# Kernel optimization log

Hardware: AMD Instinct MI355X
Metric: run time of the kernel (lower is better)

## Reference

```python
import jax, jax.numpy as jnp
import numpy as np

B, K, W, H = 32, 64, 100, 150
ALPHA = 0.2        # leaky-relu slope
THRES = 2e-4       # causal threshold


def setup_inputs() -> dict:
    ks = jax.random.split(jax.random.key(0), 20)
    s = 0.1
    inp = {
        "x": jax.random.normal(ks[0], (B, K, W), jnp.float32),
        "y": jax.random.normal(ks[1], (B, K, 1), jnp.float32),
        "z_noise": jax.random.normal(ks[2], (B, H), jnp.float32),
        "lin_w": jax.random.normal(ks[3], (W, W), jnp.float32) * s,
        "lin_b": jax.random.normal(ks[4], (W,), jnp.float32) * s,
        "a": jax.random.normal(ks[5], (2, 1), jnp.float32),
        "bias": jax.random.normal(ks[6], (K, K * W), jnp.float32) * 0.01,
        "gl_wih": jax.random.normal(ks[7], (3 * H, W), jnp.float32) * s,
        "gl_whh": jax.random.normal(ks[8], (3 * H, H), jnp.float32) * s,
        "gl_bih": jax.random.normal(ks[9], (3 * H,), jnp.float32) * s,
        "gl_bhh": jax.random.normal(ks[10], (3 * H,), jnp.float32) * s,
        "mu_w": jax.random.normal(ks[11], (H, H), jnp.float32) * s,
        "mu_b": jax.random.normal(ks[12], (H,), jnp.float32) * s,
        "std_w": jax.random.normal(ks[13], (H, H), jnp.float32) * s,
        "std_b": jax.random.normal(ks[14], (H,), jnp.float32) * s,
        "net_wih": jax.random.normal(ks[15], (K, 3 * H, W), jnp.float32) * s,
        "net_whh": jax.random.normal(ks[16], (K, 3 * H, H), jnp.float32) * s,
        "net_bih": jax.random.normal(ks[17], (K, 3 * H), jnp.float32) * s,
        "net_bhh": jax.random.normal(ks[18], (K, 3 * H), jnp.float32) * s,
    }
    return inp


def _gru_last(wih, whh, bih, bhh, xs, h0):
    # xs: [B, S, in], h0: [B, H] -> final hidden [B, H]. PyTorch gate order r,z,n.
    gx = jnp.einsum('bsi,gi->sbg', xs, wih) + bih  # [S, B, 3H]
    h_dim = h0.shape[-1]

    def step(h, g):
        gh = h @ whh.T + bhh
        r = jax.nn.sigmoid(g[:, :h_dim] + gh[:, :h_dim])
        z = jax.nn.sigmoid(g[:, h_dim:2 * h_dim] + gh[:, h_dim:2 * h_dim])
        n = jnp.tanh(g[:, 2 * h_dim:] + r * gh[:, 2 * h_dim:])
        return (1.0 - z) * n + z * h, None

    h_last, _ = jax.lax.scan(step, h0, gx)
    return h_last


def reference(x, y, z_noise, lin_w, lin_b, a, bias, gl_wih, gl_whh, gl_bih, gl_bhh,
              mu_w, mu_b, std_w, std_b, net_wih, net_whh, net_bih, net_bhh):
    xw = x[:, :, -W:]
    Wx = xw @ lin_w.T + lin_b                       # [B, K, W]
    v = Wx.reshape(Wx.shape[0], K * W)              # [B, K*W]
    # e = a_input @ a, where a_input[...,0]=y broadcast, a_input[...,1]=v tiled per node
    e = a[0, 0] * y + a[1, 0] * v[:, None, :] + bias  # [B, K, K*W]
    e = jax.nn.leaky_relu(e, ALPHA)
    attention = jax.nn.softmax(e, axis=2)           # dropout p=0 -> identity
    A = attention >= THRES                           # [B, K, K*W] mask
    Ax = jnp.where(A, v[:, None, :], 0.0)
    cause_x = Wx + Ax.sum(axis=2, keepdims=True)    # [B, K, W]
    # left GRU over the node dimension (seq len = K)
    h0 = jnp.zeros((cause_x.shape[0], H), cause_x.dtype)
    h_t = _gru_last(gl_wih, gl_whh, gl_bih, gl_bhh, cause_x, h0)  # [B, H]
    mu = h_t @ mu_w.T + mu_b
    log_var = h_t @ std_w.T + std_b
    sigma = jnp.exp(0.5 * log_var)
    z = mu + sigma * z_noise                        # [B, H]
    # K independent GRUs, same input Wx and same init state z -> vmap over weights
    causes = jax.vmap(lambda wi, wh, bi, bh: _gru_last(wi, wh, bi, bh, Wx, z))(
        net_wih, net_whh, net_bih, net_bhh)         # [K, B, H]
    return causes.transpose(1, 0, 2)                # [B, K, H]
```

## Files before the change

kernel.cpp:

```cpp
#include <hip/hip_runtime.h>

#define Bc 32
#define Kc 64
#define Wc 100
#define Hc 150
#define H3c 450
#define KWc 6400
#define ALPHAc 0.2f
#define THRESc 0.0002f

typedef unsigned int u32;
typedef unsigned short u16;
typedef __attribute__((ext_vector_type(8))) short short8;
typedef __attribute__((ext_vector_type(4))) float floatx4;

#define OFF_WX      0u
#define OFF_CS      204800u
#define OFF_GX      206848u
#define OFF_HT      1128448u
#define OFF_Z       1133248u

__device__ __forceinline__ float us2f(u16 u){ u32 x=((u32)u)<<16; return __uint_as_float(x); }
__device__ __forceinline__ u16 f2us(float f){
  u32 x = __float_as_uint(f);
  u32 r = (x + 0x7fffu + ((x>>16)&1u)) >> 16;
  return (u16)r;
}

__device__ __forceinline__ void lds_barrier(){
  __builtin_amdgcn_sched_barrier(0);
  asm volatile("s_waitcnt lgkmcnt(0)" ::: "memory");
  __builtin_amdgcn_s_barrier();
  __builtin_amdgcn_sched_barrier(0);
}

__global__ void wx_kernel(const float* __restrict__ x, const float* __restrict__ lin_w,
                          const float* __restrict__ lin_b, float* __restrict__ ws){
  int o = blockIdx.x*256 + threadIdx.x;
  if (o >= Bc*KWc) return;
  int i = o % Wc;
  int bk = o / Wc;
  const float4* xr = (const float4*)(x + bk*Wc);
  const float4* wr = (const float4*)(lin_w + i*Wc);
  float acc = lin_b[i];
  #pragma unroll
  for (int j=0;j<25;j++){
    float4 xv = xr[j], wv = wr[j];
    acc += xv.x*wv.x + xv.y*wv.y + xv.z*wv.z + xv.w*wv.w;
  }
  ws[OFF_WX + o] = acc;
}

__global__ void attn_kernel(const float* __restrict__ y, const float* __restrict__ a,
                            const float* __restrict__ bias, float* __restrict__ ws){
  __shared__ __align__(16) float e_l[KWc];
  __shared__ float red[4];
  int row = blockIdx.x;
  int b = row >> 6, k = row & 63;
  int tid = threadIdx.x;
  float a0 = a[0], a1 = a[1];
  float yv = y[row];
  const float4* v4  = (const float4*)(ws + OFF_WX + (size_t)b*KWc);
  const float4* br4 = (const float4*)(bias + (size_t)k*KWc);
  float4* e4 = (float4*)e_l;
  float ay = a0*yv;
  float m = -3.4e38f;
  for (int j=tid; j<KWc/4; j+=256){
    float4 vv = v4[j], bb = br4[j];
    float4 e;
    e.x = ay + a1*vv.x + bb.x; e.x = (e.x>=0.f)?e.x:ALPHAc*e.x;
    e.y = ay + a1*vv.y + bb.y; e.y = (e.y>=0.f)?e.y:ALPHAc*e.y;
    e.z = ay + a1*vv.z + bb.z; e.z = (e.z>=0.f)?e.z:ALPHAc*e.z;
    e.w = ay + a1*vv.w + bb.w; e.w = (e.w>=0.f)?e.w:ALPHAc*e.w;
    e4[j] = e;
    m = fmaxf(m, fmaxf(fmaxf(e.x,e.y), fmaxf(e.z,e.w)));
  }
  for (int o=32;o;o>>=1) m = fmaxf(m, __shfl_down(m, o));
  if ((tid&63)==0) red[tid>>6] = m;
  __syncthreads();
  m = fmaxf(fmaxf(red[0],red[1]), fmaxf(red[2],red[3]));
  __syncthreads();
  float ssum = 0.f;
  for (int j=tid; j<KWc/4; j+=256){
    float4 e = e4[j];
    ssum += __expf(e.x-m) + __expf(e.y-m) + __expf(e.z-m) + __expf(e.w-m);
  }
  for (int o=32;o;o>>=1) ssum += __shfl_down(ssum, o);
  if ((tid&63)==0) red[tid>>6] = ssum;
  __syncthreads();
  float s = red[0]+red[1]+red[2]+red[3];
  float thr = m + logf(THRESc * s);
  float cs = 0.f;
  for (int j=tid; j<KWc/4; j+=256){
    float4 e = e4[j];
    float4 vv = v4[j];
    if (e.x >= thr) cs += vv.x;
    if (e.y >= thr) cs += vv.y;
    if (e.z >= thr) cs += vv.z;
    if (e.w >= thr) cs += vv.w;
  }
  for (int o=32;o;o>>=1) cs += __shfl_down(cs, o);
  if ((tid&63)==0) red[tid>>6] = cs;
  __syncthreads();
  if (tid==0) ws[OFF_CS + row] = red[0]+red[1]+red[2]+red[3];
}

__global__ void glproj_kernel(const float* __restrict__ gl_wih, const float* __restrict__ gl_bih,
                              float* __restrict__ ws){
  int o = blockIdx.x*256 + threadIdx.x;
  if (o >= Kc*Bc*H3c) return;
  int g = o % H3c;
  int t = o / H3c;
  int b = t & 31, s = t >> 5;
  float cs = ws[OFF_CS + b*Kc + s];
  const float4* xr = (const float4*)(ws + OFF_WX + b*KWc + s*Wc);
  const float4* wr = (const float4*)(gl_wih + g*Wc);
  float acc = gl_bih[g];
  #pragma unroll
  for (int j=0;j<25;j++){
    float4 wv = wr[j], xv = xr[j];
    acc += (xv.x+cs)*wv.x + (xv.y+cs)*wv.y + (xv.z+cs)*wv.z + (xv.w+cs)*wv.w;
  }
  ws[OFF_GX + o] = acc;
}

__global__ void __launch_bounds__(512,1) glgru4_kernel(
    const float* __restrict__ gl_whh, const float* __restrict__ gl_bhh,
    float* __restrict__ ws){
  __shared__ __align__(16) u16 bF[5*16*40];
  __shared__ float g_l[480*10];
  int b0 = blockIdx.x*8;
  int tid = threadIdx.x;
  int w = tid >> 6, lane = tid & 63, quad = lane >> 4, n16 = lane & 15;

  short8 whhA[4][5];
  #pragma unroll
  for (int ti=0; ti<4; ti++){
    int tile = w*4 + ti;
    int sec = tile/10;
    int sr = (tile - sec*10)*16 + n16;
    bool rowok = (tile < 30) && (sr < Hc);
    int grow = (sec<3 ? sec : 2)*Hc + sr;
    const float* wr = gl_whh + (size_t)grow*Hc;
    #pragma unroll
    for (int c=0;c<5;c++){
      union { short8 v; u16 u[8]; } t8;
      #pragma unroll
      for (int j2=0;j2<4;j2++){
        int kk2 = c*32 + quad*8 + j2*2;
        float2 wv = (rowok && (kk2+1) < Hc) ? *(const float2*)(wr + kk2) : make_float2(0.f,0.f);
        t8.u[j2*2]   = f2us(wv.x);
        t8.u[j2*2+1] = f2us(wv.y);
      }
      whhA[ti][c] = t8.v;
    }
  }
  for (int i=tid; i<5*16*40/2; i+=512) ((u32*)bF)[i] = 0u;

  float hst[3] = {0.f,0.f,0.f};
  float bh_r[3], bh_z[3], bh_n[3];
  int tT[3], tBL[3];
  #pragma unroll
  for (int q=0;q<3;q++){
    int task = tid + q*512;
    if (task < 1200){
      int bl = task/150, t = task - bl*150;
      tT[q] = t; tBL[q] = bl;
      bh_r[q] = gl_bhh[t];
      bh_z[q] = gl_bhh[Hc+t];
      bh_n[q] = gl_bhh[2*Hc+t];
    } else { tT[q] = 0; tBL[q] = -1; }
  }

  for (int s=0;s<Kc;s++){
    lds_barrier();
    float gxr[3], gxz[3], gxn[3];
    const float* gxb = ws + OFF_GX + (size_t)(s*Bc)*H3c;
    #pragma unroll
    for (int q=0;q<3;q++){
      if (tBL[q] >= 0){
        const float* gp = gxb + (size_t)(b0+tBL[q])*H3c;
        int t = tT[q];
        gxr[q] = gp[t]; gxz[q] = gp[Hc+t]; gxn[q] = gp[2*Hc+t];
      }
    }
    const u16* bBase = bF + (size_t)n16*40 + (size_t)quad*8;
    short8 bh[5];
    #pragma unroll
    for (int c=0;c<5;c++) bh[c] = *(const short8*)(bBase + (size_t)c*640);
    floatx4 acc[4] = {{0.f,0.f,0.f,0.f},{0.f,0.f,0.f,0.f},{0.f,0.f,0.f,0.f},{0.f,0.f,0.f,0.f}};
    #pragma unroll
    for (int c=0;c<5;c++){
      #pragma unroll
      for (int ti=0;ti<4;ti++)
        acc[ti] = __builtin_amdgcn_mfma_f32_16x16x32_bf16(whhA[ti][c], bh[c], acc[ti], 0,0,0);
    }
    #pragma unroll
    for (int ti=0;ti<4;ti++){
      #pragma unroll
      for (int r=0;r<4;r++) acc[ti][r] += __shfl_xor(acc[ti][r], 8);
    }
    if (n16 < 8){
      #pragma unroll
      for (int ti=0;ti<4;ti++){
        int tile = w*4 + ti;
        if (tile < 30){
          int row0 = tile*16 + quad*4;
          float* gp = g_l + row0*10 + n16;
          #pragma unroll
          for (int r=0;r<4;r++) gp[r*10] = acc[ti][r];
        }
      }
    }
    lds_barrier();
    float grv[3], gzv[3], gnv[3];
    #pragma unroll
    for (int q=0;q<3;q++){
      if (tBL[q] >= 0){
        int t = tT[q], bl = tBL[q];
        grv[q] = g_l[t*10+bl];
        gzv[q] = g_l[(160+t)*10+bl];
        gnv[q] = g_l[(320+t)*10+bl];
      }
    }
    #pragma unroll
    for (int q=0;q<3;q++){
      if (tBL[q] >= 0){
        int t = tT[q], bl = tBL[q];
        float a_r = gxr[q] + grv[q] + bh_r[q];
        float a_z = gxz[q] + gzv[q] + bh_z[q];
        float r  = 1.f/(1.f+__expf(-a_r));
        float zz = 1.f/(1.f+__expf(-a_z));
        float nx = gxn[q] + r*(gnv[q] + bh_n[q]);
        nx = fminf(fmaxf(nx,-15.f),15.f);
        float e2 = __expf(2.f*nx);
        float n = (e2-1.f)/(e2+1.f);
        float h = (1.f-zz)*n + zz*hst[q];
        hst[q] = h;
        u16 hi = f2us(h); float hif = us2f(hi); u16 lo = f2us(h - hif);
        bF[(t>>5)*640 + bl*40 + (t&31)] = hi;
        bF[(t>>5)*640 + (bl+8)*40 + (t&31)] = lo;
      }
    }
  }
  #pragma unroll
  for (int q=0;q<3;q++){
    if (tBL[q] >= 0)
      ws[OFF_HT + (size_t)(b0+tBL[q])*Hc + tT[q]] = hst[q];
  }
}

__global__ void z_kernel(const float* __restrict__ z_noise, const float* __restrict__ mu_w,
                         const float* __restrict__ mu_b, const float* __restrict__ std_w,
                         const float* __restrict__ std_b, float* __restrict__ ws){
  int o = blockIdx.x*256 + threadIdx.x;
  if (o >= Bc*Hc) return;
  int t = o % Hc, b = o / Hc;
  const float* h = ws + OFF_HT + b*Hc;
  const float2* mwr = (const float2*)(mu_w + t*Hc);
  const float2* swr = (const float2*)(std_w + t*Hc);
  float mu = mu_b[t], lv = std_b[t];
  for (int j=0;j<Hc/2;j++){
    float2 mw = mwr[j], sw = swr[j];
    float h0 = h[2*j], h1 = h[2*j+1];
    mu += h0*mw.x + h1*mw.y;
    lv += h0*sw.x + h1*sw.y;
  }
  float sg = expf(0.5f*lv);
  ws[OFF_Z + o] = mu + sg*z_noise[o];
}

__global__ void __launch_bounds__(512,1) causes3_kernel(
    const float* __restrict__ net_wih, const float* __restrict__ net_whh,
    const float* __restrict__ net_bih, const float* __restrict__ net_bhh,
    const float* __restrict__ ws, float* __restrict__ out){
  __shared__ __align__(16) u16 bF[9*16*40];
  __shared__ float g_rz[320*10];
  __shared__ float g_nh[160*10];
  __shared__ float g_np[160*10];
  int kk = blockIdx.x & 63, bg = blockIdx.x >> 6, b0 = bg*8;
  int tid = threadIdx.x;
  int w = tid >> 6, lane = tid & 63, quad = lane >> 4, n16 = lane & 15;
  const float* whhk = net_whh + (size_t)kk*H3c*Hc;
  const float* wihk = net_wih + (size_t)kk*H3c*Wc;
  const float* bihk = net_bih + kk*H3c;
  const float* bhhk = net_bhh + kk*H3c;

  short8 whhA[4][5], wihA[4][4];
  #pragma unroll
  for (int ti=0; ti<4; ti++){
    int tile = w*4 + ti;
    int sec = tile/10;
    int sr = (tile - sec*10)*16 + n16;
    bool rowok = (tile < 30) && (sr < Hc);
    int grow = (sec<3 ? sec : 2)*Hc + sr;
    #pragma unroll
    for (int c=0;c<5;c++){
      union { short8 v; u16 u[8]; } t8;
      #pragma unroll
      for (int j=0;j<8;j++){
        int k = c*32 + quad*8 + j;
        float v = (rowok && k < Hc) ? whhk[(size_t)grow*Hc + k] : 0.f;
        t8.u[j] = f2us(v);
      }
      whhA[ti][c] = t8.v;
    }
    #pragma unroll
    for (int c=0;c<4;c++){
      union { short8 v; u16 u[8]; } t8;
      #pragma unroll
      for (int j=0;j<8;j++){
        int k = c*32 + quad*8 + j;
        float v = (rowok && k < Wc) ? wihk[(size_t)grow*Wc + k] : 0.f;
        t8.u[j] = f2us(v);
      }
      wihA[ti][c] = t8.v;
    }
  }

  for (int i=tid; i<9*16*40/2; i+=512) ((u32*)bF)[i] = 0u;

  float hst[3] = {0.f,0.f,0.f};
  float brz_r[3], brz_z[3], bnh_[3], bnp_[3];
  #pragma unroll
  for (int q=0;q<3;q++){
    int task = tid + q*512;
    if (task < 1200){
      int t = task >> 3, bb = task & 7;
      float h = ws[OFF_Z + (b0+bb)*Hc + t];
      hst[q] = h;
      brz_r[q] = bhhk[t]      + bihk[t];
      brz_z[q] = bhhk[Hc+t]   + bihk[Hc+t];
      bnh_[q]  = bhhk[2*Hc+t];
      bnp_[q]  = bihk[2*Hc+t];
      u16 hi = f2us(h); float hif = us2f(hi); u16 lo = f2us(h - hif);
      bF[(t>>5)*640 + bb*40 + (t&31)] = hi;
      bF[(t>>5)*640 + (bb+8)*40 + (t&31)] = lo;
    }
  }
  for (int it=tid; it<800; it+=512){
    int bb = it/100, i = it - bb*100;
    float xv = ws[OFF_WX + (b0+bb)*KWc + i];
    bF[(5+(i>>5))*640 + bb*40 + (i&31)] = f2us(xv);
  }

  int bb0 = tid/100, i0 = tid - bb0*100;
  int it1 = tid + 512;
  int bb1 = it1/100, i1 = it1 - bb1*100;
  bool v1ok = (it1 < 800);

  const bool isN = (w >= 5);
  for (int s=0;s<Kc;s++){
    float xp0 = 0.f, xp1 = 0.f;
    if (s < Kc-1){
      xp0 = ws[OFF_WX + (size_t)(b0+bb0)*KWc + (s+1)*Wc + i0];
      if (v1ok) xp1 = ws[OFF_WX + (size_t)(b0+bb1)*KWc + (s+1)*Wc + i1];
    }
    lds_barrier();
    const u16* bBase = bF + (size_t)n16*40 + (size_t)quad*8;
    short8 bx[4];
    #pragma unroll
    for (int c=0;c<4;c++) bx[c] = *(const short8*)(bBase + (size_t)(5+c)*640);
    short8 bh[5];
    #pragma unroll
    for (int c=0;c<5;c++) bh[c] = *(const short8*)(bBase + (size_t)c*640);
    floatx4 acc[4] = {{0.f,0.f,0.f,0.f},{0.f,0.f,0.f,0.f},{0.f,0.f,0.f,0.f},{0.f,0.f,0.f,0.f}};
    #pragma unroll
    for (int ca=0;ca<4;ca++){
      #pragma unroll
      for (int ti=0;ti<4;ti++)
        acc[ti] = __builtin_amdgcn_mfma_f32_16x16x32_bf16(wihA[ti][ca], bx[ca], acc[ti], 0,0,0);
    }
    if (isN){
      if (n16 < 8){
        #pragma unroll
        for (int ti=0;ti<4;ti++){
          int tile = w*4 + ti;
          if (tile < 30){
            int srb = (tile - 20)*16 + quad*4;
            float* gq = g_np + srb*10 + n16;
            #pragma unroll
            for (int r=0;r<4;r++) gq[r*10] = acc[ti][r];
          }
        }
      }
      #pragma unroll
      for (int ti=0;ti<4;ti++) acc[ti] = (floatx4){0.f,0.f,0.f,0.f};
    }
    #pragma unroll
    for (int c=0;c<5;c++){
      #pragma unroll
      for (int ti=0;ti<4;ti++)
        acc[ti] = __builtin_amdgcn_mfma_f32_16x16x32_bf16(whhA[ti][c], bh[c], acc[ti], 0,0,0);
    }
    #pragma unroll
    for (int ti=0;ti<4;ti++){
      #pragma unroll
      for (int r=0;r<4;r++) acc[ti][r] += __shfl_xor(acc[ti][r], 8);
    }
    if (n16 < 8){
      #pragma unroll
      for (int ti=0;ti<4;ti++){
        int tile = w*4 + ti;
        if (tile < 30){
          int sec = tile/10;
          int srb = (tile - sec*10)*16 + quad*4;
          if (sec < 2){
            float* gp = g_rz + (sec*160 + srb)*10 + n16;
            #pragma unroll
            for (int r=0;r<4;r++) gp[r*10] = acc[ti][r];
          } else {
            float* gh = g_nh + srb*10 + n16;
            #pragma unroll
            for (int r=0;r<4;r++) gh[r*10] = acc[ti][r];
          }
        }
      }
    }
    lds_barrier();
    #pragma unroll
    for (int q=0;q<3;q++){
      int task = tid + q*512;
      if (task < 1200){
        int t = task >> 3, bb = task & 7;
        float a_r = g_rz[t*10+bb] + brz_r[q];
        float a_z = g_rz[(160+t)*10+bb] + brz_z[q];
        float r  = 1.f/(1.f+__expf(-a_r));
        float zz = 1.f/(1.f+__expf(-a_z));
        float nx = (g_np[t*10+bb] + bnp_[q]) + r*(g_nh[t*10+bb] + bnh_[q]);
        nx = fminf(fmaxf(nx,-15.f),15.f);
        float e2 = __expf(2.f*nx);
        float n = (e2-1.f)/(e2+1.f);
        float h = (1.f-zz)*n + zz*hst[q];
        hst[q] = h;
        u16 hi = f2us(h); float hif = us2f(hi); u16 lo = f2us(h - hif);
        bF[(t>>5)*640 + bb*40 + (t&31)] = hi;
        bF[(t>>5)*640 + (bb+8)*40 + (t&31)] = lo;
      }
    }
    if (s < Kc-1){
      bF[(5+(i0>>5))*640 + bb0*40 + (i0&31)] = f2us(xp0);
      if (v1ok) bF[(5+(i1>>5))*640 + bb1*40 + (i1&31)] = f2us(xp1);
    }
  }
  #pragma unroll
  for (int q=0;q<3;q++){
    int task = tid + q*512;
    if (task < 1200){
      int t = task >> 3, bb = task & 7;
      out[((size_t)(b0+bb)*Kc + kk)*Hc + t] = hst[q];
    }
  }
}

extern "C" void kernel_launch(void* const* d_in, const int* in_sizes, int n_in,
                              void* d_out, int out_size, void* d_ws, size_t ws_size,
                              hipStream_t stream){
  const float* x        = (const float*)d_in[0];
  const float* y        = (const float*)d_in[1];
  const float* z_noise  = (const float*)d_in[2];
  const float* lin_w    = (const float*)d_in[3];
  const float* lin_b    = (const float*)d_in[4];
  const float* a        = (const float*)d_in[5];
  const float* bias     = (const float*)d_in[6];
  const float* gl_wih   = (const float*)d_in[7];
  const float* gl_whh   = (const float*)d_in[8];
  const float* gl_bih   = (const float*)d_in[9];
  const float* gl_bhh   = (const float*)d_in[10];
  const float* mu_w     = (const float*)d_in[11];
  const float* mu_b     = (const float*)d_in[12];
  const float* std_w    = (const float*)d_in[13];
  const float* std_b    = (const float*)d_in[14];
  const float* net_wih  = (const float*)d_in[15];
  const float* net_whh  = (const float*)d_in[16];
  const float* net_bih  = (const float*)d_in[17];
  const float* net_bhh  = (const float*)d_in[18];
  float* ws = (float*)d_ws;
  float* out = (float*)d_out;

  wx_kernel<<<(Bc*KWc+255)/256, 256, 0, stream>>>(x, lin_w, lin_b, ws);
  attn_kernel<<<Bc*Kc, 256, 0, stream>>>(y, a, bias, ws);
  glproj_kernel<<<(Kc*Bc*H3c+255)/256, 256, 0, stream>>>(gl_wih, gl_bih, ws);
  glgru4_kernel<<<4, 512, 0, stream>>>(gl_whh, gl_bhh, ws);
  z_kernel<<<(Bc*Hc+255)/256, 256, 0, stream>>>(z_noise, mu_w, mu_b, std_w, std_b, ws);
  causes3_kernel<<<Kc*4, 512, 0, stream>>>(net_wih, net_whh, net_bih, net_bhh, ws, out);
}
```

Before: 488.7 us.

## Rewrite left GRU recurrence as one block per batch with register-resident weights

Replaces the 4-block MFMA-based left GRU, where each block handles 8 batches with hi/lo bf16 split hidden state, with 32 blocks of one batch each. Each of 450 threads keeps one bf16 row of W_hh packed in registers and computes its dot product against an fp32 hidden state held in double-buffered LDS. The aim is to spread the serial 64-step recurrence across more CUs and shorten the per-step critical path. In exchange, the matrix cores are no longer used, each thread carries 75 registers of weights, and the weight loads are repeated per batch.

```diff
diff --git a/kernel.cpp b/kernel.cpp
--- a/kernel.cpp
+++ b/kernel.cpp
@@ -127,127 +127,71 @@
 __global__ void __launch_bounds__(512,1) glgru4_kernel(
     const float* __restrict__ gl_whh, const float* __restrict__ gl_bhh,
     float* __restrict__ ws){
-  __shared__ __align__(16) u16 bF[5*16*40];
-  __shared__ float g_l[480*10];
-  int b0 = blockIdx.x*8;
+  __shared__ __align__(16) float hbuf[2][152];
+  __shared__ float dotb[3*152];
+  int b = blockIdx.x;
   int tid = threadIdx.x;
-  int w = tid >> 6, lane = tid & 63, quad = lane >> 4, n16 = lane & 15;
-
-  short8 whhA[4][5];
-  #pragma unroll
-  for (int ti=0; ti<4; ti++){
-    int tile = w*4 + ti;
-    int sec = tile/10;
-    int sr = (tile - sec*10)*16 + n16;
-    bool rowok = (tile < 30) && (sr < Hc);
-    int grow = (sec<3 ? sec : 2)*Hc + sr;
-    const float* wr = gl_whh + (size_t)grow*Hc;
-    #pragma unroll
-    for (int c=0;c<5;c++){
-      union { short8 v; u16 u[8]; } t8;
-      #pragma unroll
-      for (int j2=0;j2<4;j2++){
-        int kk2 = c*32 + quad*8 + j2*2;
-        float2 wv = (rowok && (kk2+1) < Hc) ? *(const float2*)(wr + kk2) : make_float2(0.f,0.f);
-        t8.u[j2*2]   = f2us(wv.x);
-        t8.u[j2*2+1] = f2us(wv.y);
-      }
-      whhA[ti][c] = t8.v;
-    }
-  }
-  for (int i=tid; i<5*16*40/2; i+=512) ((u32*)bF)[i] = 0u;
-
-  float hst[3] = {0.f,0.f,0.f};
-  float bh_r[3], bh_z[3], bh_n[3];
-  int tT[3], tBL[3];
-  #pragma unroll
-  for (int q=0;q<3;q++){
-    int task = tid + q*512;
-    if (task < 1200){
-      int bl = task/150, t = task - bl*150;
-      tT[q] = t; tBL[q] = bl;
-      bh_r[q] = gl_bhh[t];
-      bh_z[q] = gl_bhh[Hc+t];
-      bh_n[q] = gl_bhh[2*Hc+t];
-    } else { tT[q] = 0; tBL[q] = -1; }
-  }
+  bool dotter = (tid < 450);
+  int g = dotter ? tid/150 : 0;
+  int t = dotter ? (tid - g*150) : 0;
+
+  u32 wreg[75];
+  {
+    const float* wr = gl_whh + (size_t)(g*Hc + t)*Hc;
+    #pragma unroll
+    for (int k2=0;k2<75;k2++){
+      float2 wv = dotter ? *(const float2*)(wr + 2*k2) : make_float2(0.f,0.f);
+      wreg[k2] = (u32)f2us(wv.x) | ((u32)f2us(wv.y) << 16);
+    }
+  }
+  if (tid < 152){ hbuf[0][tid] = 0.f; hbuf[1][tid] = 0.f; }
+
+  float bh_r=0.f, bh_z=0.f, bh_n=0.f, hreg=0.f;
+  if (tid < Hc){
+    bh_r = gl_bhh[tid]; bh_z = gl_bhh[Hc+tid]; bh_n = gl_bhh[2*Hc+tid];
+  }
+  __syncthreads();
 
   for (int s=0;s<Kc;s++){
+    int rb = s & 1;
+    float gxr=0.f, gxz=0.f, gxn=0.f;
+    if (tid < Hc){
+      const float* gp = ws + OFF_GX + (size_t)(s*Bc + b)*H3c;
+      gxr = gp[tid]; gxz = gp[Hc+tid]; gxn = gp[2*Hc+tid];
+    }
+    if (dotter){
+      const float* hb = hbuf[rb];
+      float a0=0.f, a1=0.f, a2=0.f;
+      #pragma unroll
+      for (int k2=0;k2<75;k2+=3){
+        u32 u0 = wreg[k2], u1 = wreg[k2+1], u2 = wreg[k2+2];
+        float2 h0 = *(const float2*)(hb + 2*k2);
+        float2 h1 = *(const float2*)(hb + 2*k2+2);
+        float2 h2 = *(const float2*)(hb + 2*k2+4);
+        a0 += __uint_as_float(u0<<16)*h0.x + __uint_as_float(u0&0xffff0000u)*h0.y;
+        a1 += __uint_as_float(u1<<16)*h1.x + __uint_as_float(u1&0xffff0000u)*h1.y;
+        a2 += __uint_as_float(u2<<16)*h2.x + __uint_as_float(u2&0xffff0000u)*h2.y;
+      }
+      dotb[g*152 + t] = a0 + a1 + a2;
+    }
     lds_barrier();
-    float gxr[3], gxz[3], gxn[3];
-    const float* gxb = ws + OFF_GX + (size_t)(s*Bc)*H3c;
-    #pragma unroll
-    for (int q=0;q<3;q++){
-      if (tBL[q] >= 0){
-        const float* gp = gxb + (size_t)(b0+tBL[q])*H3c;
-        int t = tT[q];
-        gxr[q] = gp[t]; gxz[q] = gp[Hc+t]; gxn[q] = gp[2*Hc+t];
-      }
-    }
-    const u16* bBase = bF + (size_t)n16*40 + (size_t)quad*8;
-    short8 bh[5];
-    #pragma unroll
-    for (int c=0;c<5;c++) bh[c] = *(const short8*)(bBase + (size_t)c*640);
-    floatx4 acc[4] = {{0.f,0.f,0.f,0.f},{0.f,0.f,0.f,0.f},{0.f,0.f,0.f,0.f},{0.f,0.f,0.f,0.f}};
-    #pragma unroll
-    for (int c=0;c<5;c++){
-      #pragma unroll
-      for (int ti=0;ti<4;ti++)
-        acc[ti] = __builtin_amdgcn_mfma_f32_16x16x32_bf16(whhA[ti][c], bh[c], acc[ti], 0,0,0);
-    }
-    #pragma unroll
-    for (int ti=0;ti<4;ti++){
-      #pragma unroll
-      for (int r=0;r<4;r++) acc[ti][r] += __shfl_xor(acc[ti][r], 8);
-    }
-    if (n16 < 8){
-      #pragma unroll
-      for (int ti=0;ti<4;ti++){
-        int tile = w*4 + ti;
-        if (tile < 30){
-          int row0 = tile*16 + quad*4;
-          float* gp = g_l + row0*10 + n16;
-          #pragma unroll
-          for (int r=0;r<4;r++) gp[r*10] = acc[ti][r];
-        }
-      }
+    if (tid < Hc){
+      float a_r = gxr + dotb[tid]       + bh_r;
+      float a_z = gxz + dotb[152+tid]   + bh_z;
+      float dn  =       dotb[304+tid]   + bh_n;
+      float rr = 1.f/(1.f+__expf(-a_r));
+      float zz = 1.f/(1.f+__expf(-a_z));
+      float nx = gxn + rr*dn;
+      nx = fminf(fmaxf(nx,-15.f),15.f);
+      float e2 = __expf(2.f*nx);
+      float n = (e2-1.f)/(e2+1.f);
+      float h = (1.f-zz)*n + zz*hreg;
+      hreg = h;
+      hbuf[rb^1][tid] = h;
     }
     lds_barrier();
-    float grv[3], gzv[3], gnv[3];
-    #pragma unroll
-    for (int q=0;q<3;q++){
-      if (tBL[q] >= 0){
-        int t = tT[q], bl = tBL[q];
-        grv[q] = g_l[t*10+bl];
-        gzv[q] = g_l[(160+t)*10+bl];
-        gnv[q] = g_l[(320+t)*10+bl];
-      }
-    }
-    #pragma unroll
-    for (int q=0;q<3;q++){
-      if (tBL[q] >= 0){
-        int t = tT[q], bl = tBL[q];
-        float a_r = gxr[q] + grv[q] + bh_r[q];
-        float a_z = gxz[q] + gzv[q] + bh_z[q];
-        float r  = 1.f/(1.f+__expf(-a_r));
-        float zz = 1.f/(1.f+__expf(-a_z));
-        float nx = gxn[q] + r*(gnv[q] + bh_n[q]);
-        nx = fminf(fmaxf(nx,-15.f),15.f);
-        float e2 = __expf(2.f*nx);
-        float n = (e2-1.f)/(e2+1.f);
-        float h = (1.f-zz)*n + zz*hst[q];
-        hst[q] = h;
-        u16 hi = f2us(h); float hif = us2f(hi); u16 lo = f2us(h - hif);
-        bF[(t>>5)*640 + bl*40 + (t&31)] = hi;
-        bF[(t>>5)*640 + (bl+8)*40 + (t&31)] = lo;
-      }
-    }
-  }
-  #pragma unroll
-  for (int q=0;q<3;q++){
-    if (tBL[q] >= 0)
-      ws[OFF_HT + (size_t)(b0+tBL[q])*Hc + tT[q]] = hst[q];
-  }
+  }
+  if (tid < Hc) ws[OFF_HT + (size_t)b*Hc + tid] = hreg;
 }
 
 __global__ void z_kernel(const float* __restrict__ z_noise, const float* __restrict__ mu_w,
@@ -481,7 +425,7 @@
   wx_kernel<<<(Bc*KWc+255)/256, 256, 0, stream>>>(x, lin_w, lin_b, ws);
   attn_kernel<<<Bc*Kc, 256, 0, stream>>>(y, a, bias, ws);
   glproj_kernel<<<(Kc*Bc*H3c+255)/256, 256, 0, stream>>>(gl_wih, gl_bih, ws);
-  glgru4_kernel<<<4, 512, 0, stream>>>(gl_whh, gl_bhh, ws);
+  glgru4_kernel<<<Bc, 512, 0, stream>>>(gl_whh, gl_bhh, ws);
   z_kernel<<<(Bc*Hc+255)/256, 256, 0, stream>>>(z_noise, mu_w, mu_b, std_w, std_b, ws);
   causes3_kernel<<<Kc*4, 512, 0, stream>>>(net_wih, net_whh, net_bih, net_bhh, ws, out);
 }
```

After: 483.8 us. Within noise of the previous version (-1.0%).
